# Kernel tuning notes

Hardware: AMD Instinct MI355X
Metric: run time of the kernel (lower is better)

Reference implementation:

```python
import jax, jax.numpy as jnp
import numpy as np

N_NODES = 100000


def gcn_conv(x, src, dst, loops, W, b):
    """PyG-style GCNConv: add self-loops, sym-normalize, linear, scatter-add."""
    h = x @ W  # [N, out]
    s = jnp.concatenate([src, loops])
    d = jnp.concatenate([dst, loops])
    deg = jax.ops.segment_sum(jnp.ones(s.shape, h.dtype), d, num_segments=N_NODES)
    dinv = jnp.where(deg > 0, deg ** -0.5, 0.0)
    norm = dinv[s] * dinv[d]  # [E+N]
    out = jax.ops.segment_sum(h[s] * norm[:, None], d, num_segments=N_NODES)
    return out + b


def setup_inputs() -> dict:
    key = jax.random.key(0)
    ks = jax.random.split(key, 12)
    num_classes, nf = 10, 3
    x = jax.random.normal(ks[0], (N_NODES, nf), jnp.float32)
    edge_index = jax.random.randint(ks[1], (2, 3200000), 0, N_NODES, jnp.int64)

    def lin(k, fi, fo):
        k1, k2 = jax.random.split(k)
        lim = 1.0 / np.sqrt(fi)
        W = jax.random.uniform(k1, (fi, fo), jnp.float32, -lim, lim)
        b = jax.random.uniform(k2, (fo,), jnp.float32, -lim, lim)
        return W, b

    W1, b1 = lin(ks[2], nf, 16)
    W2, b2 = lin(ks[3], 16, 3)
    W3, b3 = lin(ks[4], 3, 3)
    Wp, bp = lin(ks[5], 3, 3)
    Wl, bl = lin(ks[6], 3, num_classes)
    return {"x": x, "edge_index": edge_index, "W1": W1, "b1": b1, "W2": W2,
            "b2": b2, "W3": W3, "b3": b3, "Wp": Wp, "bp": bp, "Wl": Wl, "bl": bl}


def reference(x, edge_index, W1, b1, W2, b2, W3, b3, Wp, bp, Wl, bl):
    src, dst = edge_index[0], edge_index[1]
    loops = jnp.arange(N_NODES, dtype=edge_index.dtype)

    h = gcn_conv(x, src, dst, loops, W1, b1)
    h = jax.nn.relu(h)
    h = gcn_conv(h, src, dst, loops, W2, b2)
    # F.normalize (L2, dim=1, eps=1e-12)
    nrm = jnp.maximum(jnp.linalg.norm(h, axis=1, keepdims=True), 1e-12)
    h = h / nrm
    embed_1 = jax.lax.stop_gradient(h)
    h = gcn_conv(h, src, dst, loops, W3, b3)
    h = h @ Wp + bp  # project
    pooled = jnp.mean(h, axis=0, keepdims=True)  # global_mean_pool, batch=None -> [1,3]
    logits = pooled @ Wl + bl
    return jax.nn.log_softmax(logits, axis=1), (h, embed_1)
```

## Files before the change

### kernel.cpp

```cpp
#include <hip/hip_runtime.h>
#include <math.h>

#define N_NODES 100000
#define NB 256
#define NP 256
#define BSH 9
#define BMASK 511u
#define G 8


__global__ void k_hist(const int* __restrict__ dst, int E,
                       int* __restrict__ hist) {
    __shared__ int bin[NP];
    if (threadIdx.x < NP) bin[threadIdx.x] = 0;
    __syncthreads();
    int ngroups = E >> 2;
    int gchunk = (ngroups + NB - 1) / NB;
    int gbeg = blockIdx.x * gchunk;
    int gend = gbeg + gchunk; if (gend > ngroups) gend = ngroups;
    const int4* d4 = (const int4*)dst;
    for (int g = gbeg + threadIdx.x; g < gend; g += 1024) {
        int4 d = d4[g];
        atomicAdd(&bin[d.x >> BSH], 1);
        atomicAdd(&bin[d.y >> BSH], 1);
        atomicAdd(&bin[d.z >> BSH], 1);
        atomicAdd(&bin[d.w >> BSH], 1);
    }
    if (blockIdx.x == 0) {
        for (int e = (ngroups << 2) + threadIdx.x; e < E; e += 1024)
            atomicAdd(&bin[dst[e] >> BSH], 1);
    }
    __syncthreads();
    if (threadIdx.x < NP)
        hist[blockIdx.x * NP + threadIdx.x] = bin[threadIdx.x];
}

__global__ void k_s1(const int* __restrict__ hist, int* __restrict__ base) {
    __shared__ int sh[NP];
    int b = threadIdx.x;
    int s = 0;
    #pragma unroll 8
    for (int k = 0; k < NB; ++k) s += hist[k * NP + b];
    sh[b] = s;
    __syncthreads();
    for (int off = 1; off < NP; off <<= 1) {
        int u = (b >= off) ? sh[b - off] : 0;
        __syncthreads();
        sh[b] += u;
        __syncthreads();
    }
    base[b] = sh[b] - s;
    if (b == NP - 1) base[NP] = sh[b];
}

__global__ void k_s2(int* __restrict__ hist, const int* __restrict__ base) {
    __shared__ int sh[NB];
    int b = blockIdx.x, t = threadIdx.x;
    int v = hist[t * NP + b];
    sh[t] = v;
    __syncthreads();
    for (int off = 1; off < NB; off <<= 1) {
        int u = (t >= off) ? sh[t - off] : 0;
        __syncthreads();
        sh[t] += u;
        __syncthreads();
    }
    hist[t * NP + b] = base[b] + sh[t] - v;
}

__global__ void k_part(const int* __restrict__ src, const int* __restrict__ dst,
                       int E, const int* __restrict__ hist,
                       unsigned int* __restrict__ part) {
    __shared__ int cur[NP];
    if (threadIdx.x < NP)
        cur[threadIdx.x] = hist[blockIdx.x * NP + threadIdx.x];
    __syncthreads();
    int ngroups = E >> 2;
    int gchunk = (ngroups + NB - 1) / NB;
    int gbeg = blockIdx.x * gchunk;
    int gend = gbeg + gchunk; if (gend > ngroups) gend = ngroups;
    const int4* d4 = (const int4*)dst;
    const int4* s4 = (const int4*)src;
    for (int g = gbeg + threadIdx.x; g < gend; g += 1024) {
        int4 d = d4[g];
        int4 s = s4[g];
        int p;
        p = atomicAdd(&cur[d.x >> BSH], 1);
        part[p] = ((unsigned)s.x << BSH) | ((unsigned)d.x & BMASK);
        p = atomicAdd(&cur[d.y >> BSH], 1);
        part[p] = ((unsigned)s.y << BSH) | ((unsigned)d.y & BMASK);
        p = atomicAdd(&cur[d.z >> BSH], 1);
        part[p] = ((unsigned)s.z << BSH) | ((unsigned)d.z & BMASK);
        p = atomicAdd(&cur[d.w >> BSH], 1);
        part[p] = ((unsigned)s.w << BSH) | ((unsigned)d.w & BMASK);
    }
    if (blockIdx.x == 0) {
        for (int e = (ngroups << 2) + threadIdx.x; e < E; e += 1024) {
            int d = dst[e];
            int p = atomicAdd(&cur[d >> BSH], 1);
            part[p] = ((unsigned)src[e] << BSH) | ((unsigned)d & BMASK);
        }
    }
}

__global__ void k_csr(const unsigned int* __restrict__ part, const int* __restrict__ base,
                      const float* __restrict__ x,
                      int* __restrict__ offs,
                      float4* __restrict__ xp4, int* __restrict__ col, int N) {
    __shared__ int cnt[512];
    __shared__ int scn[512];
    __shared__ int cur[512];
    int b = blockIdx.x, t = threadIdx.x;
    int lo = base[b], hi = base[b + 1];
    if (t < 512) cnt[t] = 0;
    __syncthreads();
    for (int e = lo + t; e < hi; e += 1024)
        atomicAdd(&cnt[part[e] & BMASK], 1);
    __syncthreads();
    int v = (t < 512) ? cnt[t] : 0;
    if (t < 512) scn[t] = v;
    __syncthreads();
    for (int off = 1; off < 512; off <<= 1) {
        int u = (t < 512 && t >= off) ? scn[t - off] : 0;
        __syncthreads();
        if (t < 512) scn[t] += u;
        __syncthreads();
    }
    if (t < 512) {
        int pos = lo + scn[t] - v;
        cur[t] = pos;
        int g = (b << BSH) + t;
        if (g < N) {
            offs[g] = pos;
            float di = rsqrtf((float)(v + 1));
            xp4[g] = make_float4(x[3*g] * di, x[3*g+1] * di, x[3*g+2] * di, di);
        }
    }
    if (b == 0 && t == 0) offs[N] = base[(N_NODES + 511) >> BSH];
    __syncthreads();
    for (int e = lo + t; e < hi; e += 1024) {
        unsigned int w = part[e];
        int p = atomicAdd(&cur[w & BMASK], 1);
        col[p] = (int)(w >> BSH);
    }
}


__global__ void k_deg(const int* __restrict__ dst, int E, int* __restrict__ deg) {
    int e = blockIdx.x * blockDim.x + threadIdx.x;
    if (e < E) atomicAdd(&deg[dst[e]], 1);
}

__global__ void k_scan1(const int* __restrict__ deg, int* __restrict__ offs,
                        int* __restrict__ partl, int N) {
    __shared__ int sh[256];
    int i = blockIdx.x * 256 + threadIdx.x;
    int t = threadIdx.x;
    int v = (i < N) ? deg[i] : 0;
    sh[t] = v;
    __syncthreads();
    #pragma unroll
    for (int off = 1; off < 256; off <<= 1) {
        int u = (t >= off) ? sh[t - off] : 0;
        __syncthreads();
        sh[t] += u;
        __syncthreads();
    }
    if (i < N) offs[i] = sh[t] - v;
    if (t == 255) partl[blockIdx.x] = sh[255];
}

__global__ void k_scan2(int* __restrict__ partl, int* __restrict__ offs, int nb, int N) {
    __shared__ int sh[1024];
    int t = threadIdx.x;
    int v = (t < nb) ? partl[t] : 0;
    sh[t] = v;
    __syncthreads();
    #pragma unroll
    for (int off = 1; off < 1024; off <<= 1) {
        int u = (t >= off) ? sh[t - off] : 0;
        __syncthreads();
        sh[t] += u;
        __syncthreads();
    }
    if (t < nb) partl[t] = sh[t] - v;
    if (t == 1023) offs[N] = sh[1023];
}

__global__ void k_scan3(int* __restrict__ offs, const int* __restrict__ partl, int N) {
    int i = blockIdx.x * 256 + threadIdx.x;
    if (i < N) offs[i] += partl[blockIdx.x];
}

__global__ void k_fill_cur(const int* __restrict__ src, const int* __restrict__ dst,
                           const int* __restrict__ offs, int* __restrict__ cur,
                           int* __restrict__ col, int E) {
    int e = blockIdx.x * blockDim.x + threadIdx.x;
    if (e >= E) return;
    int d = dst[e];
    col[offs[d] + atomicAdd(&cur[d], 1)] = src[e];
}

__global__ void k_prescale(const float* __restrict__ x, const int* __restrict__ offs,
                           float4* __restrict__ xp4, int N) {
    int i = blockIdx.x * blockDim.x + threadIdx.x;
    if (i >= N) return;
    int d = offs[i+1] - offs[i];
    float di = rsqrtf((float)(d + 1));
    xp4[i] = make_float4(x[3*i] * di, x[3*i+1] * di, x[3*i+2] * di, di);
}


__device__ __forceinline__ void gather_sum(const int* __restrict__ col,
                                           const float4* __restrict__ tab,
                                           int beg, int end, int g,
                                           float& s0, float& s1, float& s2) {
    int k = beg + g;
    for (; k + 3*G < end; k += 4*G) {
        int c0 = col[k], c1 = col[k+G], c2 = col[k+2*G], c3 = col[k+3*G];
        float4 v0 = tab[c0], v1 = tab[c1], v2 = tab[c2], v3 = tab[c3];
        s0 += v0.x; s1 += v0.y; s2 += v0.z;
        s0 += v1.x; s1 += v1.y; s2 += v1.z;
        s0 += v2.x; s1 += v2.y; s2 += v2.z;
        s0 += v3.x; s1 += v3.y; s2 += v3.z;
    }
    for (; k < end; k += G) {
        float4 v = tab[col[k]];
        s0 += v.x; s1 += v.y; s2 += v.z;
    }
}

__global__ void k_conv1(const int* __restrict__ offs, const int* __restrict__ col,
                        const float4* __restrict__ xp4,
                        const float* __restrict__ W1, const float* __restrict__ b1,
                        const float* __restrict__ W2,
                        float4* __restrict__ h2p4, int N) {
    int tid = blockIdx.x * blockDim.x + threadIdx.x;
    int i = tid >> 3, g = tid & (G - 1);
    if (i >= N) return;
    float s0 = 0.f, s1 = 0.f, s2 = 0.f, di = 0.f;
    if (g == 0) {
        float4 self = xp4[i];
        s0 = self.x; s1 = self.y; s2 = self.z; di = self.w;
    }
    gather_sum(col, xp4, offs[i], offs[i+1], g, s0, s1, s2);
    #pragma unroll
    for (int off = G/2; off > 0; off >>= 1) {
        s0 += __shfl_down(s0, off, G);
        s1 += __shfl_down(s1, off, G);
        s2 += __shfl_down(s2, off, G);
    }
    if (g == 0) {
        float g0 = s0 * di, g1 = s1 * di, g2 = s2 * di;
        float o0 = 0.f, o1 = 0.f, o2 = 0.f;
        #pragma unroll
        for (int j = 0; j < 16; ++j) {
            float t = fmaxf(g0 * W1[j] + g1 * W1[16 + j] + g2 * W1[32 + j] + b1[j], 0.f);
            o0 += t * W2[3*j + 0];
            o1 += t * W2[3*j + 1];
            o2 += t * W2[3*j + 2];
        }
        h2p4[i] = make_float4(o0 * di, o1 * di, o2 * di, di);
    }
}

__global__ void k_conv2(const int* __restrict__ offs, const int* __restrict__ col,
                        const float4* __restrict__ h2p4,
                        const float* __restrict__ b2, const float* __restrict__ W3,
                        float* __restrict__ embed_out, float4* __restrict__ h3p4, int N) {
    int tid = blockIdx.x * blockDim.x + threadIdx.x;
    int i = tid >> 3, g = tid & (G - 1);
    if (i >= N) return;
    float s0 = 0.f, s1 = 0.f, s2 = 0.f, di = 0.f;
    if (g == 0) {
        float4 self = h2p4[i];
        s0 = self.x; s1 = self.y; s2 = self.z; di = self.w;
    }
    gather_sum(col, h2p4, offs[i], offs[i+1], g, s0, s1, s2);
    #pragma unroll
    for (int off = G/2; off > 0; off >>= 1) {
        s0 += __shfl_down(s0, off, G);
        s1 += __shfl_down(s1, off, G);
        s2 += __shfl_down(s2, off, G);
    }
    if (g == 0) {
        float t0 = s0 * di + b2[0];
        float t1 = s1 * di + b2[1];
        float t2 = s2 * di + b2[2];
        float inv = 1.0f / fmaxf(sqrtf(t0*t0 + t1*t1 + t2*t2), 1e-12f);
        float e0 = t0*inv, e1 = t1*inv, e2 = t2*inv;
        embed_out[3*i] = e0; embed_out[3*i+1] = e1; embed_out[3*i+2] = e2;
        h3p4[i] = make_float4((e0*W3[0] + e1*W3[3] + e2*W3[6]) * di,
                              (e0*W3[1] + e1*W3[4] + e2*W3[7]) * di,
                              (e0*W3[2] + e1*W3[5] + e2*W3[8]) * di, di);
    }
}

__global__ void k_conv3(const int* __restrict__ offs, const int* __restrict__ col,
                        const float4* __restrict__ h3p4,
                        const float* __restrict__ b3, const float* __restrict__ Wp,
                        const float* __restrict__ bp,
                        float* __restrict__ hout, float* __restrict__ pool, int N) {
    __shared__ float ws[4][3];
    int tid = blockIdx.x * blockDim.x + threadIdx.x;
    int i = tid >> 3, g = tid & (G - 1);
    float p0 = 0.f, p1 = 0.f, p2 = 0.f;
    if (i < N) {
        float s0 = 0.f, s1 = 0.f, s2 = 0.f, di = 0.f;
        if (g == 0) {
            float4 self = h3p4[i];
            s0 = self.x; s1 = self.y; s2 = self.z; di = self.w;
        }
        gather_sum(col, h3p4, offs[i], offs[i+1], g, s0, s1, s2);
        #pragma unroll
        for (int off = G/2; off > 0; off >>= 1) {
            s0 += __shfl_down(s0, off, G);
            s1 += __shfl_down(s1, off, G);
            s2 += __shfl_down(s2, off, G);
        }
        if (g == 0) {
            float t0 = s0 * di + b3[0];
            float t1 = s1 * di + b3[1];
            float t2 = s2 * di + b3[2];
            p0 = t0*Wp[0] + t1*Wp[3] + t2*Wp[6] + bp[0];
            p1 = t0*Wp[1] + t1*Wp[4] + t2*Wp[7] + bp[1];
            p2 = t0*Wp[2] + t1*Wp[5] + t2*Wp[8] + bp[2];
            hout[3*i] = p0; hout[3*i+1] = p1; hout[3*i+2] = p2;
        }
    }
    #pragma unroll
    for (int off = 32; off > 0; off >>= 1) {
        p0 += __shfl_down(p0, off);
        p1 += __shfl_down(p1, off);
        p2 += __shfl_down(p2, off);
    }
    if ((threadIdx.x & 63) == 0) {
        int w = threadIdx.x >> 6;
        ws[w][0] = p0; ws[w][1] = p1; ws[w][2] = p2;
    }
    __syncthreads();
    if (threadIdx.x == 0) {
        pool[3*blockIdx.x]   = ws[0][0] + ws[1][0] + ws[2][0] + ws[3][0];
        pool[3*blockIdx.x+1] = ws[0][1] + ws[1][1] + ws[2][1] + ws[3][1];
        pool[3*blockIdx.x+2] = ws[0][2] + ws[1][2] + ws[2][2] + ws[3][2];
    }
}

__global__ void k_head(const float* __restrict__ pool, int nb,
                       const float* __restrict__ Wl, const float* __restrict__ bl,
                       float* __restrict__ out, int N) {
    __shared__ float sh[12];
    int t = threadIdx.x;
    float p0 = 0.f, p1 = 0.f, p2 = 0.f;
    for (int k = t; k < nb; k += 256) {
        p0 += pool[3*k]; p1 += pool[3*k+1]; p2 += pool[3*k+2];
    }
    #pragma unroll
    for (int off = 32; off > 0; off >>= 1) {
        p0 += __shfl_down(p0, off);
        p1 += __shfl_down(p1, off);
        p2 += __shfl_down(p2, off);
    }
    if ((t & 63) == 0) {
        int w = t >> 6;
        sh[3*w] = p0; sh[3*w+1] = p1; sh[3*w+2] = p2;
    }
    __syncthreads();
    if (t == 0) {
        p0 = sh[0] + sh[3] + sh[6] + sh[9];
        p1 = sh[1] + sh[4] + sh[7] + sh[10];
        p2 = sh[2] + sh[5] + sh[8] + sh[11];
        p0 /= (float)N; p1 /= (float)N; p2 /= (float)N;
        float l[10];
        float m = -1e30f;
        #pragma unroll
        for (int j = 0; j < 10; ++j) {
            l[j] = p0 * Wl[j] + p1 * Wl[10 + j] + p2 * Wl[20 + j] + bl[j];
            m = fmaxf(m, l[j]);
        }
        float s = 0.f;
        #pragma unroll
        for (int j = 0; j < 10; ++j) s += expf(l[j] - m);
        float lse = logf(s) + m;
        #pragma unroll
        for (int j = 0; j < 10; ++j) out[j] = l[j] - lse;
    }
}

extern "C" void kernel_launch(void* const* d_in, const int* in_sizes, int n_in,
                              void* d_out, int out_size, void* d_ws, size_t ws_size,
                              hipStream_t stream) {
    const int N = N_NODES;
    const float* x  = (const float*)d_in[0];
    const int*   ei = (const int*)d_in[1];
    const int    E  = in_sizes[1] / 2;
    const int* src = ei;
    const int* dst = ei + E;
    const float* W1 = (const float*)d_in[2];
    const float* b1 = (const float*)d_in[3];
    const float* W2 = (const float*)d_in[4];
    const float* b2 = (const float*)d_in[5];
    const float* W3 = (const float*)d_in[6];
    const float* b3 = (const float*)d_in[7];
    const float* Wp = (const float*)d_in[8];
    const float* bp = (const float*)d_in[9];
    const float* Wl = (const float*)d_in[10];
    const float* bl = (const float*)d_in[11];

    float* out     = (float*)d_out;
    float* h_out   = out + 10;
    float* emb_out = out + 10 + 3 * N;

    const int B = 256;
    int gE = (E + B - 1) / B;
    int gN = (N + B - 1) / B;
    int gC = ((size_t)N * G + B - 1) / B;
    int PB = (N + 511) >> BSH;

    char* Wm = (char*)d_ws;

    size_t off = 0;
    auto alloc = [&](size_t elems) { void* p = Wm + off; off += elems * 4; return p; };
    int*          col  = (int*)alloc((size_t)E);
    unsigned int* part = (unsigned int*)alloc((size_t)E);
    int*          hist = (int*)alloc((size_t)NB * NP);
    int*          base = (int*)alloc(NP + 1);
    int*          offs = (int*)alloc(N + 1);
    float4*       bufA = (float4*)alloc(4 * N);
    float4*       bufB = (float4*)alloc(4 * N);
    float*        pool = (float*)alloc(3 * (size_t)gC + 4);
    size_t need_bucket = off;

    if (ws_size >= need_bucket) {
        k_hist<<<NB, 1024, 0, stream>>>(dst, E, hist);
        k_s1<<<1, NP, 0, stream>>>(hist, base);
        k_s2<<<NP, NB, 0, stream>>>(hist, base);
        k_part<<<NB, 1024, 0, stream>>>(src, dst, E, hist, part);
        k_csr<<<PB, 1024, 0, stream>>>(part, base, x, offs, bufA, col, N);
    } else {
        off = 0;
        col  = (int*)alloc((size_t)E);
        int* deg = (int*)alloc(N);
        offs = (int*)alloc(N + 1);
        bufA = (float4*)alloc(4 * N);
        bufB = (float4*)alloc(4 * N);
        pool = (float*)alloc(3 * (size_t)gC + 4);
        int* partl = (int*)alloc(1024);
        int* cur = (int*)alloc(N);

        hipMemsetAsync(deg, 0, N * sizeof(int), stream);
        hipMemsetAsync(cur, 0, N * sizeof(int), stream);

        k_deg<<<gE, B, 0, stream>>>(dst, E, deg);
        k_scan1<<<gN, B, 0, stream>>>(deg, offs, partl, N);
        k_scan2<<<1, 1024, 0, stream>>>(partl, offs, gN, N);
        k_scan3<<<gN, B, 0, stream>>>(offs, partl, N);
        k_fill_cur<<<gE, B, 0, stream>>>(src, dst, offs, cur, col, E);
        k_prescale<<<gN, B, 0, stream>>>(x, offs, bufA, N);
    }

    k_conv1<<<gC, B, 0, stream>>>(offs, col, bufA, W1, b1, W2, bufB, N);
    k_conv2<<<gC, B, 0, stream>>>(offs, col, bufB, b2, W3, emb_out, bufA, N);
    k_conv3<<<gC, B, 0, stream>>>(offs, col, bufA, b3, Wp, bp, h_out, pool, N);

    k_head<<<1, 256, 0, stream>>>(pool, gC, Wl, bl, out, N);
}
```

Baseline: 134.7 us.

## Replace per-node CSR build with bucket-wise LDS scatter-accumulate over partitioned edges

Drops the second counting-sort pass that built the per-node CSR (col/offs). Each of the three conv layers now streams the bucket-partitioned edge words directly and accumulates neighbor features into shared memory with LDS float atomics, one block per 256-node bucket. Bucket width is halved (256 nodes, 512 partitions) so the accumulators fit in LDS, and a vec_ok fallback is added for unaligned inputs. In exchange, three layers of heavy shared-memory atomics replace register-level gather sums, and the summation order becomes nondeterministic.

Result: slower. 255.7 us (+89.9%).

```diff
diff --git a/kernel.cpp b/kernel.cpp
--- a/kernel.cpp
+++ b/kernel.cpp
@@ -1,33 +1,44 @@
 #include <hip/hip_runtime.h>
 #include <math.h>
+#include <stdint.h>
 
 #define N_NODES 100000
 #define NB 256
-#define NP 256
-#define BSH 9
-#define BMASK 511u
+#define NP 512
+#define BSH 8
+#define BMASK 255u
+#define NPB 256
+#define TC 512
 #define G 8
 
 
-__global__ void k_hist(const int* __restrict__ dst, int E,
+__global__ void k_hist(const int* __restrict__ dst, int E, int vec_ok,
                        int* __restrict__ hist) {
     __shared__ int bin[NP];
     if (threadIdx.x < NP) bin[threadIdx.x] = 0;
     __syncthreads();
-    int ngroups = E >> 2;
-    int gchunk = (ngroups + NB - 1) / NB;
-    int gbeg = blockIdx.x * gchunk;
-    int gend = gbeg + gchunk; if (gend > ngroups) gend = ngroups;
-    const int4* d4 = (const int4*)dst;
-    for (int g = gbeg + threadIdx.x; g < gend; g += 1024) {
-        int4 d = d4[g];
-        atomicAdd(&bin[d.x >> BSH], 1);
-        atomicAdd(&bin[d.y >> BSH], 1);
-        atomicAdd(&bin[d.z >> BSH], 1);
-        atomicAdd(&bin[d.w >> BSH], 1);
-    }
-    if (blockIdx.x == 0) {
-        for (int e = (ngroups << 2) + threadIdx.x; e < E; e += 1024)
+    if (vec_ok) {
+        int ngroups = E >> 2;
+        int gchunk = (ngroups + NB - 1) / NB;
+        int gbeg = blockIdx.x * gchunk;
+        int gend = gbeg + gchunk; if (gend > ngroups) gend = ngroups;
+        const int4* d4 = (const int4*)dst;
+        for (int g = gbeg + threadIdx.x; g < gend; g += 1024) {
+            int4 d = d4[g];
+            atomicAdd(&bin[d.x >> BSH], 1);
+            atomicAdd(&bin[d.y >> BSH], 1);
+            atomicAdd(&bin[d.z >> BSH], 1);
+            atomicAdd(&bin[d.w >> BSH], 1);
+        }
+        if (blockIdx.x == 0) {
+            for (int e = (ngroups << 2) + threadIdx.x; e < E; e += 1024)
+                atomicAdd(&bin[dst[e] >> BSH], 1);
+        }
+    } else {
+        int echunk = (E + NB - 1) / NB;
+        int ebeg = blockIdx.x * echunk;
+        int eend = ebeg + echunk; if (eend > E) eend = E;
+        for (int e = ebeg + threadIdx.x; e < eend; e += 1024)
             atomicAdd(&bin[dst[e] >> BSH], 1);
     }
     __syncthreads();
@@ -35,7 +46,7 @@
         hist[blockIdx.x * NP + threadIdx.x] = bin[threadIdx.x];
 }
 
-__global__ void k_s1(const int* __restrict__ hist, int* __restrict__ base) {
+__global__ void k_s1(const int* __restrict__ hist, int* __restrict__ base, int E) {
     __shared__ int sh[NP];
     int b = threadIdx.x;
     int s = 0;
@@ -50,7 +61,7 @@
         __syncthreads();
     }
     base[b] = sh[b] - s;
-    if (b == NP - 1) base[NP] = sh[b];
+    if (b == NP - 1) base[NP] = E;
 }
 
 __global__ void k_s2(int* __restrict__ hist, const int* __restrict__ base) {
@@ -69,33 +80,44 @@
 }
 
 __global__ void k_part(const int* __restrict__ src, const int* __restrict__ dst,
-                       int E, const int* __restrict__ hist,
+                       int E, int vec_ok, const int* __restrict__ hist,
                        unsigned int* __restrict__ part) {
     __shared__ int cur[NP];
     if (threadIdx.x < NP)
         cur[threadIdx.x] = hist[blockIdx.x * NP + threadIdx.x];
     __syncthreads();
-    int ngroups = E >> 2;
-    int gchunk = (ngroups + NB - 1) / NB;
-    int gbeg = blockIdx.x * gchunk;
-    int gend = gbeg + gchunk; if (gend > ngroups) gend = ngroups;
-    const int4* d4 = (const int4*)dst;
-    const int4* s4 = (const int4*)src;
-    for (int g = gbeg + threadIdx.x; g < gend; g += 1024) {
-        int4 d = d4[g];
-        int4 s = s4[g];
-        int p;
-        p = atomicAdd(&cur[d.x >> BSH], 1);
-        part[p] = ((unsigned)s.x << BSH) | ((unsigned)d.x & BMASK);
-        p = atomicAdd(&cur[d.y >> BSH], 1);
-        part[p] = ((unsigned)s.y << BSH) | ((unsigned)d.y & BMASK);
-        p = atomicAdd(&cur[d.z >> BSH], 1);
-        part[p] = ((unsigned)s.z << BSH) | ((unsigned)d.z & BMASK);
-        p = atomicAdd(&cur[d.w >> BSH], 1);
-        part[p] = ((unsigned)s.w << BSH) | ((unsigned)d.w & BMASK);
-    }
-    if (blockIdx.x == 0) {
-        for (int e = (ngroups << 2) + threadIdx.x; e < E; e += 1024) {
+    if (vec_ok) {
+        int ngroups = E >> 2;
+        int gchunk = (ngroups + NB - 1) / NB;
+        int gbeg = blockIdx.x * gchunk;
+        int gend = gbeg + gchunk; if (gend > ngroups) gend = ngroups;
+        const int4* d4 = (const int4*)dst;
+        const int4* s4 = (const int4*)src;
+        for (int g = gbeg + threadIdx.x; g < gend; g += 1024) {
+            int4 d = d4[g];
+            int4 s = s4[g];
+            int p;
+            p = atomicAdd(&cur[d.x >> BSH], 1);
+            part[p] = ((unsigned)s.x << BSH) | ((unsigned)d.x & BMASK);
+            p = atomicAdd(&cur[d.y >> BSH], 1);
+            part[p] = ((unsigned)s.y << BSH) | ((unsigned)d.y & BMASK);
+            p = atomicAdd(&cur[d.z >> BSH], 1);
+            part[p] = ((unsigned)s.z << BSH) | ((unsigned)d.z & BMASK);
+            p = atomicAdd(&cur[d.w >> BSH], 1);
+            part[p] = ((unsigned)s.w << BSH) | ((unsigned)d.w & BMASK);
+        }
+        if (blockIdx.x == 0) {
+            for (int e = (ngroups << 2) + threadIdx.x; e < E; e += 1024) {
+                int d = dst[e];
+                int p = atomicAdd(&cur[d >> BSH], 1);
+                part[p] = ((unsigned)src[e] << BSH) | ((unsigned)d & BMASK);
+            }
+        }
+    } else {
+        int echunk = (E + NB - 1) / NB;
+        int ebeg = blockIdx.x * echunk;
+        int eend = ebeg + echunk; if (eend > E) eend = E;
+        for (int e = ebeg + threadIdx.x; e < eend; e += 1024) {
             int d = dst[e];
             int p = atomicAdd(&cur[d >> BSH], 1);
             part[p] = ((unsigned)src[e] << BSH) | ((unsigned)d & BMASK);
@@ -103,45 +125,202 @@
     }
 }
 
-__global__ void k_csr(const unsigned int* __restrict__ part, const int* __restrict__ base,
-                      const float* __restrict__ x,
-                      int* __restrict__ offs,
-                      float4* __restrict__ xp4, int* __restrict__ col, int N) {
-    __shared__ int cnt[512];
-    __shared__ int scn[512];
-    __shared__ int cur[512];
+__global__ __launch_bounds__(TC) void k_pre(const unsigned int* __restrict__ part,
+                                            const int* __restrict__ base,
+                                            const float* __restrict__ x,
+                                            float4* __restrict__ xp4, int N) {
+    __shared__ int cnt[NPB];
     int b = blockIdx.x, t = threadIdx.x;
+    if (t < NPB) cnt[t] = 0;
+    __syncthreads();
     int lo = base[b], hi = base[b + 1];
-    if (t < 512) cnt[t] = 0;
-    __syncthreads();
-    for (int e = lo + t; e < hi; e += 1024)
+    for (int e = lo + t; e < hi; e += TC)
         atomicAdd(&cnt[part[e] & BMASK], 1);
     __syncthreads();
-    int v = (t < 512) ? cnt[t] : 0;
-    if (t < 512) scn[t] = v;
-    __syncthreads();
-    for (int off = 1; off < 512; off <<= 1) {
-        int u = (t < 512 && t >= off) ? scn[t - off] : 0;
-        __syncthreads();
-        if (t < 512) scn[t] += u;
-        __syncthreads();
-    }
-    if (t < 512) {
-        int pos = lo + scn[t] - v;
-        cur[t] = pos;
-        int g = (b << BSH) + t;
-        if (g < N) {
-            offs[g] = pos;
-            float di = rsqrtf((float)(v + 1));
-            xp4[g] = make_float4(x[3*g] * di, x[3*g+1] * di, x[3*g+2] * di, di);
-        }
-    }
-    if (b == 0 && t == 0) offs[N] = base[(N_NODES + 511) >> BSH];
-    __syncthreads();
-    for (int e = lo + t; e < hi; e += 1024) {
-        unsigned int w = part[e];
-        int p = atomicAdd(&cur[w & BMASK], 1);
-        col[p] = (int)(w >> BSH);
+    if (t < NPB) {
+        int node = (b << BSH) + t;
+        if (node < N) {
+            float di = rsqrtf((float)(cnt[t] + 1));
+            xp4[node] = make_float4(x[3*node] * di, x[3*node+1] * di,
+                                    x[3*node+2] * di, di);
+        }
+    }
+}
+
+
+#define ACC3(w, f, v) atomicAdd(&acc[3*((w) & BMASK) + (f)], (v))
+
+__device__ __forceinline__ void bucket_accum(const unsigned int* __restrict__ part,
+                                             const float4* __restrict__ tab,
+                                             float* acc, int lo, int hi, int t) {
+    int e = lo + t;
+    for (; e + 7*TC < hi; e += 8*TC) {
+        unsigned w0 = part[e],      w1 = part[e+TC],   w2 = part[e+2*TC], w3 = part[e+3*TC];
+        unsigned w4 = part[e+4*TC], w5 = part[e+5*TC], w6 = part[e+6*TC], w7 = part[e+7*TC];
+        float4 v0 = tab[w0 >> BSH], v1 = tab[w1 >> BSH], v2 = tab[w2 >> BSH], v3 = tab[w3 >> BSH];
+        float4 v4 = tab[w4 >> BSH], v5 = tab[w5 >> BSH], v6 = tab[w6 >> BSH], v7 = tab[w7 >> BSH];
+        ACC3(w0,0,v0.x); ACC3(w0,1,v0.y); ACC3(w0,2,v0.z);
+        ACC3(w1,0,v1.x); ACC3(w1,1,v1.y); ACC3(w1,2,v1.z);
+        ACC3(w2,0,v2.x); ACC3(w2,1,v2.y); ACC3(w2,2,v2.z);
+        ACC3(w3,0,v3.x); ACC3(w3,1,v3.y); ACC3(w3,2,v3.z);
+        ACC3(w4,0,v4.x); ACC3(w4,1,v4.y); ACC3(w4,2,v4.z);
+        ACC3(w5,0,v5.x); ACC3(w5,1,v5.y); ACC3(w5,2,v5.z);
+        ACC3(w6,0,v6.x); ACC3(w6,1,v6.y); ACC3(w6,2,v6.z);
+        ACC3(w7,0,v7.x); ACC3(w7,1,v7.y); ACC3(w7,2,v7.z);
+    }
+    for (; e < hi; e += TC) {
+        unsigned w = part[e];
+        float4 v = tab[w >> BSH];
+        ACC3(w,0,v.x); ACC3(w,1,v.y); ACC3(w,2,v.z);
+    }
+}
+
+__global__ __launch_bounds__(TC) void k_sc1(const unsigned int* __restrict__ part,
+        const int* __restrict__ base, const float4* __restrict__ xp4,
+        const float* __restrict__ W1, const float* __restrict__ b1,
+        const float* __restrict__ W2, float4* __restrict__ h2p4, int N) {
+    __shared__ float acc[NPB * 3];
+    int b = blockIdx.x, t = threadIdx.x;
+    int node = (b << BSH) + t;
+    float4 self = make_float4(0.f, 0.f, 0.f, 0.f);
+    if (t < NPB) {
+        if (node < N) self = xp4[node];
+        acc[3*t] = self.x; acc[3*t+1] = self.y; acc[3*t+2] = self.z;
+    }
+    __syncthreads();
+    bucket_accum(part, xp4, acc, base[b], base[b+1], t);
+    __syncthreads();
+    if (t < NPB && node < N) {
+        float di = self.w;
+        float g0 = acc[3*t] * di, g1 = acc[3*t+1] * di, g2 = acc[3*t+2] * di;
+        float o0 = 0.f, o1 = 0.f, o2 = 0.f;
+        #pragma unroll
+        for (int j = 0; j < 16; ++j) {
+            float tv = fmaxf(g0 * W1[j] + g1 * W1[16 + j] + g2 * W1[32 + j] + b1[j], 0.f);
+            o0 += tv * W2[3*j + 0];
+            o1 += tv * W2[3*j + 1];
+            o2 += tv * W2[3*j + 2];
+        }
+        h2p4[node] = make_float4(o0 * di, o1 * di, o2 * di, di);
+    }
+}
+
+__global__ __launch_bounds__(TC) void k_sc2(const unsigned int* __restrict__ part,
+        const int* __restrict__ base, const float4* __restrict__ h2p4,
+        const float* __restrict__ b2, const float* __restrict__ W3,
+        float* __restrict__ embed_out, float4* __restrict__ h3p4, int N) {
+    __shared__ float acc[NPB * 3];
+    int b = blockIdx.x, t = threadIdx.x;
+    int node = (b << BSH) + t;
+    float4 self = make_float4(0.f, 0.f, 0.f, 0.f);
+    if (t < NPB) {
+        if (node < N) self = h2p4[node];
+        acc[3*t] = self.x; acc[3*t+1] = self.y; acc[3*t+2] = self.z;
+    }
+    __syncthreads();
+    bucket_accum(part, h2p4, acc, base[b], base[b+1], t);
+    __syncthreads();
+    if (t < NPB && node < N) {
+        float di = self.w;
+        float t0 = acc[3*t]   * di + b2[0];
+        float t1 = acc[3*t+1] * di + b2[1];
+        float t2 = acc[3*t+2] * di + b2[2];
+        float inv = 1.0f / fmaxf(sqrtf(t0*t0 + t1*t1 + t2*t2), 1e-12f);
+        float e0 = t0*inv, e1 = t1*inv, e2 = t2*inv;
+        embed_out[3*node] = e0; embed_out[3*node+1] = e1; embed_out[3*node+2] = e2;
+        h3p4[node] = make_float4((e0*W3[0] + e1*W3[3] + e2*W3[6]) * di,
+                                 (e0*W3[1] + e1*W3[4] + e2*W3[7]) * di,
+                                 (e0*W3[2] + e1*W3[5] + e2*W3[8]) * di, di);
+    }
+}
+
+__global__ __launch_bounds__(TC) void k_sc3(const unsigned int* __restrict__ part,
+        const int* __restrict__ base, const float4* __restrict__ h3p4,
+        const float* __restrict__ b3, const float* __restrict__ Wp,
+        const float* __restrict__ bp,
+        float* __restrict__ hout, float* __restrict__ pool, int N) {
+    __shared__ float acc[NPB * 3];
+    __shared__ float wsum[TC/64][3];
+    int b = blockIdx.x, t = threadIdx.x;
+    int node = (b << BSH) + t;
+    float4 self = make_float4(0.f, 0.f, 0.f, 0.f);
+    if (t < NPB) {
+        if (node < N) self = h3p4[node];
+        acc[3*t] = self.x; acc[3*t+1] = self.y; acc[3*t+2] = self.z;
+    }
+    __syncthreads();
+    bucket_accum(part, h3p4, acc, base[b], base[b+1], t);
+    __syncthreads();
+    float q0 = 0.f, q1 = 0.f, q2 = 0.f;
+    if (t < NPB && node < N) {
+        float di = self.w;
+        float t0 = acc[3*t]   * di + b3[0];
+        float t1 = acc[3*t+1] * di + b3[1];
+        float t2 = acc[3*t+2] * di + b3[2];
+        q0 = t0*Wp[0] + t1*Wp[3] + t2*Wp[6] + bp[0];
+        q1 = t0*Wp[1] + t1*Wp[4] + t2*Wp[7] + bp[1];
+        q2 = t0*Wp[2] + t1*Wp[5] + t2*Wp[8] + bp[2];
+        hout[3*node] = q0; hout[3*node+1] = q1; hout[3*node+2] = q2;
+    }
+    #pragma unroll
+    for (int off = 32; off > 0; off >>= 1) {
+        q0 += __shfl_down(q0, off);
+        q1 += __shfl_down(q1, off);
+        q2 += __shfl_down(q2, off);
+    }
+    if ((t & 63) == 0) {
+        int w = t >> 6;
+        wsum[w][0] = q0; wsum[w][1] = q1; wsum[w][2] = q2;
+    }
+    __syncthreads();
+    if (t == 0) {
+        float a0 = 0.f, a1 = 0.f, a2 = 0.f;
+        #pragma unroll
+        for (int w = 0; w < TC/64; ++w) {
+            a0 += wsum[w][0]; a1 += wsum[w][1]; a2 += wsum[w][2];
+        }
+        pool[3*b] = a0; pool[3*b+1] = a1; pool[3*b+2] = a2;
+    }
+}
+
+__global__ void k_head(const float* __restrict__ pool, int nb,
+                       const float* __restrict__ Wl, const float* __restrict__ bl,
+                       float* __restrict__ out, int N) {
+    __shared__ float sh[12];
+    int t = threadIdx.x;
+    float p0 = 0.f, p1 = 0.f, p2 = 0.f;
+    for (int k = t; k < nb; k += 256) {
+        p0 += pool[3*k]; p1 += pool[3*k+1]; p2 += pool[3*k+2];
+    }
+    #pragma unroll
+    for (int off = 32; off > 0; off >>= 1) {
+        p0 += __shfl_down(p0, off);
+        p1 += __shfl_down(p1, off);
+        p2 += __shfl_down(p2, off);
+    }
+    if ((t & 63) == 0) {
+        int w = t >> 6;
+        sh[3*w] = p0; sh[3*w+1] = p1; sh[3*w+2] = p2;
+    }
+    __syncthreads();
+    if (t == 0) {
+        p0 = sh[0] + sh[3] + sh[6] + sh[9];
+        p1 = sh[1] + sh[4] + sh[7] + sh[10];
+        p2 = sh[2] + sh[5] + sh[8] + sh[11];
+        p0 /= (float)N; p1 /= (float)N; p2 /= (float)N;
+        float l[10];
+        float m = -1e30f;
+        #pragma unroll
+        for (int j = 0; j < 10; ++j) {
+            l[j] = p0 * Wl[j] + p1 * Wl[10 + j] + p2 * Wl[20 + j] + bl[j];
+            m = fmaxf(m, l[j]);
+        }
+        float s = 0.f;
+        #pragma unroll
+        for (int j = 0; j < 10; ++j) s += expf(l[j] - m);
+        float lse = logf(s) + m;
+        #pragma unroll
+        for (int j = 0; j < 10; ++j) out[j] = l[j] - lse;
     }
 }
 
@@ -209,7 +388,6 @@
     float di = rsqrtf((float)(d + 1));
     xp4[i] = make_float4(x[3*i] * di, x[3*i+1] * di, x[3*i+2] * di, di);
 }
-
 
 __device__ __forceinline__ void gather_sum(const int* __restrict__ col,
                                            const float4* __restrict__ tab,
@@ -343,47 +521,6 @@
         pool[3*blockIdx.x]   = ws[0][0] + ws[1][0] + ws[2][0] + ws[3][0];
         pool[3*blockIdx.x+1] = ws[0][1] + ws[1][1] + ws[2][1] + ws[3][1];
         pool[3*blockIdx.x+2] = ws[0][2] + ws[1][2] + ws[2][2] + ws[3][2];
-    }
-}
-
-__global__ void k_head(const float* __restrict__ pool, int nb,
-                       const float* __restrict__ Wl, const float* __restrict__ bl,
-                       float* __restrict__ out, int N) {
-    __shared__ float sh[12];
-    int t = threadIdx.x;
-    float p0 = 0.f, p1 = 0.f, p2 = 0.f;
-    for (int k = t; k < nb; k += 256) {
-        p0 += pool[3*k]; p1 += pool[3*k+1]; p2 += pool[3*k+2];
-    }
-    #pragma unroll
-    for (int off = 32; off > 0; off >>= 1) {
-        p0 += __shfl_down(p0, off);
-        p1 += __shfl_down(p1, off);
-        p2 += __shfl_down(p2, off);
-    }
-    if ((t & 63) == 0) {
-        int w = t >> 6;
-        sh[3*w] = p0; sh[3*w+1] = p1; sh[3*w+2] = p2;
-    }
-    __syncthreads();
-    if (t == 0) {
-        p0 = sh[0] + sh[3] + sh[6] + sh[9];
-        p1 = sh[1] + sh[4] + sh[7] + sh[10];
-        p2 = sh[2] + sh[5] + sh[8] + sh[11];
-        p0 /= (float)N; p1 /= (float)N; p2 /= (float)N;
-        float l[10];
-        float m = -1e30f;
-        #pragma unroll
-        for (int j = 0; j < 10; ++j) {
-            l[j] = p0 * Wl[j] + p1 * Wl[10 + j] + p2 * Wl[20 + j] + bl[j];
-            m = fmaxf(m, l[j]);
-        }
-        float s = 0.f;
-        #pragma unroll
-        for (int j = 0; j < 10; ++j) s += expf(l[j] - m);
-        float lse = logf(s) + m;
-        #pragma unroll
-        for (int j = 0; j < 10; ++j) out[j] = l[j] - lse;
     }
 }
 
@@ -411,57 +548,65 @@
     float* h_out   = out + 10;
     float* emb_out = out + 10 + 3 * N;
 
-    const int B = 256;
-    int gE = (E + B - 1) / B;
-    int gN = (N + B - 1) / B;
-    int gC = ((size_t)N * G + B - 1) / B;
-    int PB = (N + 511) >> BSH;
+    const int NBUCK = (N + NPB - 1) >> BSH;
 
     char* Wm = (char*)d_ws;
-
     size_t off = 0;
     auto alloc = [&](size_t elems) { void* p = Wm + off; off += elems * 4; return p; };
-    int*          col  = (int*)alloc((size_t)E);
+
     unsigned int* part = (unsigned int*)alloc((size_t)E);
     int*          hist = (int*)alloc((size_t)NB * NP);
     int*          base = (int*)alloc(NP + 1);
-    int*          offs = (int*)alloc(N + 1);
     float4*       bufA = (float4*)alloc(4 * N);
     float4*       bufB = (float4*)alloc(4 * N);
-    float*        pool = (float*)alloc(3 * (size_t)gC + 4);
+    float*        pool = (float*)alloc(3 * NP + 4);
     size_t need_bucket = off;
 
+    int vec_ok = ((E & 3) == 0) &&
+                 ((((uintptr_t)dst) & 15) == 0) &&
+                 ((((uintptr_t)src) & 15) == 0);
+
     if (ws_size >= need_bucket) {
-        k_hist<<<NB, 1024, 0, stream>>>(dst, E, hist);
-        k_s1<<<1, NP, 0, stream>>>(hist, base);
+        k_hist<<<NB, 1024, 0, stream>>>(dst, E, vec_ok, hist);
+        k_s1<<<1, NP, 0, stream>>>(hist, base, E);
         k_s2<<<NP, NB, 0, stream>>>(hist, base);
-        k_part<<<NB, 1024, 0, stream>>>(src, dst, E, hist, part);
-        k_csr<<<PB, 1024, 0, stream>>>(part, base, x, offs, bufA, col, N);
+        k_part<<<NB, 1024, 0, stream>>>(src, dst, E, vec_ok, hist, part);
+        k_pre<<<NBUCK, TC, 0, stream>>>(part, base, x, bufA, N);
+
+        k_sc1<<<NBUCK, TC, 0, stream>>>(part, base, bufA, W1, b1, W2, bufB, N);
+        k_sc2<<<NBUCK, TC, 0, stream>>>(part, base, bufB, b2, W3, emb_out, bufA, N);
+        k_sc3<<<NBUCK, TC, 0, stream>>>(part, base, bufA, b3, Wp, bp, h_out, pool, N);
+
+        k_head<<<1, 256, 0, stream>>>(pool, NBUCK, Wl, bl, out, N);
     } else {
         off = 0;
-        col  = (int*)alloc((size_t)E);
-        int* deg = (int*)alloc(N);
-        offs = (int*)alloc(N + 1);
-        bufA = (float4*)alloc(4 * N);
-        bufB = (float4*)alloc(4 * N);
-        pool = (float*)alloc(3 * (size_t)gC + 4);
-        int* partl = (int*)alloc(1024);
-        int* cur = (int*)alloc(N);
+        int*    col  = (int*)alloc((size_t)E);
+        int*    deg  = (int*)alloc(N);
+        int*    offs = (int*)alloc(N + 1);
+        float4* fA   = (float4*)alloc(4 * N);
+        float4* fB   = (float4*)alloc(4 * N);
+        int gC = ((size_t)N * G + 255) / 256;
+        float*  fpool = (float*)alloc(3 * (size_t)gC + 4);
+        int*    partl = (int*)alloc(1024);
+        int*    cur   = (int*)alloc(N);
 
         hipMemsetAsync(deg, 0, N * sizeof(int), stream);
         hipMemsetAsync(cur, 0, N * sizeof(int), stream);
+
+        const int B = 256;
+        int gE = (E + B - 1) / B;
+        int gN = (N + B - 1) / B;
 
         k_deg<<<gE, B, 0, stream>>>(dst, E, deg);
         k_scan1<<<gN, B, 0, stream>>>(deg, offs, partl, N);
         k_scan2<<<1, 1024, 0, stream>>>(partl, offs, gN, N);
         k_scan3<<<gN, B, 0, stream>>>(offs, partl, N);
         k_fill_cur<<<gE, B, 0, stream>>>(src, dst, offs, cur, col, E);
-        k_prescale<<<gN, B, 0, stream>>>(x, offs, bufA, N);
-    }
-
-    k_conv1<<<gC, B, 0, stream>>>(offs, col, bufA, W1, b1, W2, bufB, N);
-    k_conv2<<<gC, B, 0, stream>>>(offs, col, bufB, b2, W3, emb_out, bufA, N);
-    k_conv3<<<gC, B, 0, stream>>>(offs, col, bufA, b3, Wp, bp, h_out, pool, N);
-
-    k_head<<<1, 256, 0, stream>>>(pool, gC, Wl, bl, out, N);
-}
+        k_prescale<<<gN, B, 0, stream>>>(x, offs, fA, N);
+
+        k_conv1<<<gC, B, 0, stream>>>(offs, col, fA, W1, b1, W2, fB, N);
+        k_conv2<<<gC, B, 0, stream>>>(offs, col, fB, b2, W3, emb_out, fA, N);
+        k_conv3<<<gC, B, 0, stream>>>(offs, col, fA, b3, Wp, bp, h_out, fpool, N);
+        k_head<<<1, 256, 0, stream>>>(fpool, gC, Wl, bl, out, N);
+    }
+}
```

## Use nontemporal gather loads, rebalance bucket blocks, add scalar fallback path

Applied to the files above, without the earlier changes.

Doubles the number of histogram/partition blocks to 512 while halving threads per block to 512, which spreads the edge stream across more workgroups. It adds a scalar fallback for cases where E is not a multiple of four or the edge pointers are misaligned, and sets the bucket total directly to E. The gather loads in the aggregation kernels now use nontemporal loads, meant to reduce cache pollution from the random feature-table reads. The trade-offs are a larger hist array and more work in the scan stage, and nontemporal hints may hurt reuse of the small feature table, which could otherwise stay resident in cache.

After: 200.4 us. 1.49x slower.

```diff
diff --git a/kernel.cpp b/kernel.cpp
--- a/kernel.cpp
+++ b/kernel.cpp
@@ -1,33 +1,43 @@
 #include <hip/hip_runtime.h>
 #include <math.h>
+#include <stdint.h>
 
 #define N_NODES 100000
-#define NB 256
+#define NB 512
+#define TPP 512
 #define NP 256
 #define BSH 9
 #define BMASK 511u
 #define G 8
 
 
-__global__ void k_hist(const int* __restrict__ dst, int E,
+__global__ void k_hist(const int* __restrict__ dst, int E, int vec_ok,
                        int* __restrict__ hist) {
     __shared__ int bin[NP];
     if (threadIdx.x < NP) bin[threadIdx.x] = 0;
     __syncthreads();
-    int ngroups = E >> 2;
-    int gchunk = (ngroups + NB - 1) / NB;
-    int gbeg = blockIdx.x * gchunk;
-    int gend = gbeg + gchunk; if (gend > ngroups) gend = ngroups;
-    const int4* d4 = (const int4*)dst;
-    for (int g = gbeg + threadIdx.x; g < gend; g += 1024) {
-        int4 d = d4[g];
-        atomicAdd(&bin[d.x >> BSH], 1);
-        atomicAdd(&bin[d.y >> BSH], 1);
-        atomicAdd(&bin[d.z >> BSH], 1);
-        atomicAdd(&bin[d.w >> BSH], 1);
-    }
-    if (blockIdx.x == 0) {
-        for (int e = (ngroups << 2) + threadIdx.x; e < E; e += 1024)
+    if (vec_ok) {
+        int ngroups = E >> 2;
+        int gchunk = (ngroups + NB - 1) / NB;
+        int gbeg = blockIdx.x * gchunk;
+        int gend = gbeg + gchunk; if (gend > ngroups) gend = ngroups;
+        const int4* d4 = (const int4*)dst;
+        for (int g = gbeg + threadIdx.x; g < gend; g += TPP) {
+            int4 d = d4[g];
+            atomicAdd(&bin[d.x >> BSH], 1);
+            atomicAdd(&bin[d.y >> BSH], 1);
+            atomicAdd(&bin[d.z >> BSH], 1);
+            atomicAdd(&bin[d.w >> BSH], 1);
+        }
+        if (blockIdx.x == 0) {
+            for (int e = (ngroups << 2) + threadIdx.x; e < E; e += TPP)
+                atomicAdd(&bin[dst[e] >> BSH], 1);
+        }
+    } else {
+        int echunk = (E + NB - 1) / NB;
+        int ebeg = blockIdx.x * echunk;
+        int eend = ebeg + echunk; if (eend > E) eend = E;
+        for (int e = ebeg + threadIdx.x; e < eend; e += TPP)
             atomicAdd(&bin[dst[e] >> BSH], 1);
     }
     __syncthreads();
@@ -35,7 +45,7 @@
         hist[blockIdx.x * NP + threadIdx.x] = bin[threadIdx.x];
 }
 
-__global__ void k_s1(const int* __restrict__ hist, int* __restrict__ base) {
+__global__ void k_s1(const int* __restrict__ hist, int* __restrict__ base, int E) {
     __shared__ int sh[NP];
     int b = threadIdx.x;
     int s = 0;
@@ -50,7 +60,7 @@
         __syncthreads();
     }
     base[b] = sh[b] - s;
-    if (b == NP - 1) base[NP] = sh[b];
+    if (b == NP - 1) base[NP] = E;
 }
 
 __global__ void k_s2(int* __restrict__ hist, const int* __restrict__ base) {
@@ -69,33 +79,44 @@
 }
 
 __global__ void k_part(const int* __restrict__ src, const int* __restrict__ dst,
-                       int E, const int* __restrict__ hist,
+                       int E, int vec_ok, const int* __restrict__ hist,
                        unsigned int* __restrict__ part) {
     __shared__ int cur[NP];
     if (threadIdx.x < NP)
         cur[threadIdx.x] = hist[blockIdx.x * NP + threadIdx.x];
     __syncthreads();
-    int ngroups = E >> 2;
-    int gchunk = (ngroups + NB - 1) / NB;
-    int gbeg = blockIdx.x * gchunk;
-    int gend = gbeg + gchunk; if (gend > ngroups) gend = ngroups;
-    const int4* d4 = (const int4*)dst;
-    const int4* s4 = (const int4*)src;
-    for (int g = gbeg + threadIdx.x; g < gend; g += 1024) {
-        int4 d = d4[g];
-        int4 s = s4[g];
-        int p;
-        p = atomicAdd(&cur[d.x >> BSH], 1);
-        part[p] = ((unsigned)s.x << BSH) | ((unsigned)d.x & BMASK);
-        p = atomicAdd(&cur[d.y >> BSH], 1);
-        part[p] = ((unsigned)s.y << BSH) | ((unsigned)d.y & BMASK);
-        p = atomicAdd(&cur[d.z >> BSH], 1);
-        part[p] = ((unsigned)s.z << BSH) | ((unsigned)d.z & BMASK);
-        p = atomicAdd(&cur[d.w >> BSH], 1);
-        part[p] = ((unsigned)s.w << BSH) | ((unsigned)d.w & BMASK);
-    }
-    if (blockIdx.x == 0) {
-        for (int e = (ngroups << 2) + threadIdx.x; e < E; e += 1024) {
+    if (vec_ok) {
+        int ngroups = E >> 2;
+        int gchunk = (ngroups + NB - 1) / NB;
+        int gbeg = blockIdx.x * gchunk;
+        int gend = gbeg + gchunk; if (gend > ngroups) gend = ngroups;
+        const int4* d4 = (const int4*)dst;
+        const int4* s4 = (const int4*)src;
+        for (int g = gbeg + threadIdx.x; g < gend; g += TPP) {
+            int4 d = d4[g];
+            int4 s = s4[g];
+            int p;
+            p = atomicAdd(&cur[d.x >> BSH], 1);
+            part[p] = ((unsigned)s.x << BSH) | ((unsigned)d.x & BMASK);
+            p = atomicAdd(&cur[d.y >> BSH], 1);
+            part[p] = ((unsigned)s.y << BSH) | ((unsigned)d.y & BMASK);
+            p = atomicAdd(&cur[d.z >> BSH], 1);
+            part[p] = ((unsigned)s.z << BSH) | ((unsigned)d.z & BMASK);
+            p = atomicAdd(&cur[d.w >> BSH], 1);
+            part[p] = ((unsigned)s.w << BSH) | ((unsigned)d.w & BMASK);
+        }
+        if (blockIdx.x == 0) {
+            for (int e = (ngroups << 2) + threadIdx.x; e < E; e += TPP) {
+                int d = dst[e];
+                int p = atomicAdd(&cur[d >> BSH], 1);
+                part[p] = ((unsigned)src[e] << BSH) | ((unsigned)d & BMASK);
+            }
+        }
+    } else {
+        int echunk = (E + NB - 1) / NB;
+        int ebeg = blockIdx.x * echunk;
+        int eend = ebeg + echunk; if (eend > E) eend = E;
+        for (int e = ebeg + threadIdx.x; e < eend; e += TPP) {
             int d = dst[e];
             int p = atomicAdd(&cur[d >> BSH], 1);
             part[p] = ((unsigned)src[e] << BSH) | ((unsigned)d & BMASK);
@@ -211,6 +232,13 @@
 }
 
 
+typedef float nat4 __attribute__((ext_vector_type(4)));
+
+__device__ __forceinline__ float4 ldnt4(const float4* p) {
+    nat4 v = __builtin_nontemporal_load((const nat4*)p);
+    return make_float4(v.x, v.y, v.z, v.w);
+}
+
 __device__ __forceinline__ void gather_sum(const int* __restrict__ col,
                                            const float4* __restrict__ tab,
                                            int beg, int end, int g,
@@ -218,14 +246,15 @@
     int k = beg + g;
     for (; k + 3*G < end; k += 4*G) {
         int c0 = col[k], c1 = col[k+G], c2 = col[k+2*G], c3 = col[k+3*G];
-        float4 v0 = tab[c0], v1 = tab[c1], v2 = tab[c2], v3 = tab[c3];
+        float4 v0 = ldnt4(&tab[c0]), v1 = ldnt4(&tab[c1]);
+        float4 v2 = ldnt4(&tab[c2]), v3 = ldnt4(&tab[c3]);
         s0 += v0.x; s1 += v0.y; s2 += v0.z;
         s0 += v1.x; s1 += v1.y; s2 += v1.z;
         s0 += v2.x; s1 += v2.y; s2 += v2.z;
         s0 += v3.x; s1 += v3.y; s2 += v3.z;
     }
     for (; k < end; k += G) {
-        float4 v = tab[col[k]];
+        float4 v = ldnt4(&tab[col[k]]);
         s0 += v.x; s1 += v.y; s2 += v.z;
     }
 }
@@ -418,9 +447,9 @@
     int PB = (N + 511) >> BSH;
 
     char* Wm = (char*)d_ws;
-
     size_t off = 0;
     auto alloc = [&](size_t elems) { void* p = Wm + off; off += elems * 4; return p; };
+
     int*          col  = (int*)alloc((size_t)E);
     unsigned int* part = (unsigned int*)alloc((size_t)E);
     int*          hist = (int*)alloc((size_t)NB * NP);
@@ -431,11 +460,15 @@
     float*        pool = (float*)alloc(3 * (size_t)gC + 4);
     size_t need_bucket = off;
 
+    int vec_ok = ((E & 3) == 0) &&
+                 ((((uintptr_t)dst) & 15) == 0) &&
+                 ((((uintptr_t)src) & 15) == 0);
+
     if (ws_size >= need_bucket) {
-        k_hist<<<NB, 1024, 0, stream>>>(dst, E, hist);
-        k_s1<<<1, NP, 0, stream>>>(hist, base);
+        k_hist<<<NB, TPP, 0, stream>>>(dst, E, vec_ok, hist);
+        k_s1<<<1, NP, 0, stream>>>(hist, base, E);
         k_s2<<<NP, NB, 0, stream>>>(hist, base);
-        k_part<<<NB, 1024, 0, stream>>>(src, dst, E, hist, part);
+        k_part<<<NB, TPP, 0, stream>>>(src, dst, E, vec_ok, hist, part);
         k_csr<<<PB, 1024, 0, stream>>>(part, base, x, offs, bufA, col, N);
     } else {
         off = 0;
```
